# Kernel optimization log

Hardware: AMD Instinct MI355X
Metric: run time of the kernel (lower is better)

## Reference

```python
import jax, jax.numpy as jnp
import numpy as np

VOCAB = 32000
EMB = 256
HID = 1024
N = 5            # n-gram order
NM1 = N - 1      # context length
PAD = 0          # pad_index (ignore_index for CE, padding_idx for embedding)


def setup_inputs() -> dict:
    key = jax.random.key(0)
    ks = jax.random.split(key, 9)
    B, S = 16, 512
    text = jax.random.randint(ks[0], (B, S), 0, VOCAB)
    target = jax.random.randint(ks[1], (B, S), 0, VOCAB)
    sc = lambda fan_in: 1.0 / np.sqrt(fan_in)
    embed = jax.random.normal(ks[2], (VOCAB, EMB), jnp.float32) * 0.02
    W1 = jax.random.uniform(ks[3], (NM1 * EMB, HID), jnp.float32, -sc(NM1 * EMB), sc(NM1 * EMB))
    b1 = jax.random.uniform(ks[4], (HID,), jnp.float32, -sc(NM1 * EMB), sc(NM1 * EMB))
    W2 = jax.random.uniform(ks[5], (HID, HID), jnp.float32, -sc(HID), sc(HID))
    b2 = jax.random.uniform(ks[6], (HID,), jnp.float32, -sc(HID), sc(HID))
    Wo = jax.random.uniform(ks[7], (HID, VOCAB), jnp.float32, -sc(HID), sc(HID))
    bo = jax.random.uniform(ks[8], (VOCAB,), jnp.float32, -sc(HID), sc(HID))
    return {"text": text, "target": target, "embed": embed,
            "W1": W1, "b1": b1, "W2": W2, "b2": b2, "Wo": Wo, "bo": bo}


def reference(text, target, embed, W1, b1, W2, b2, Wo, bo):
    B, S = text.shape
    # left-pad with PAD so contexts[:, i] == previous n-1 tokens (padded for i < n-1)
    padded = jnp.pad(text, ((0, 0), (NM1, 0)), constant_values=PAD)  # [B, S+NM1]
    win = jnp.arange(S)[:, None] + jnp.arange(NM1)[None, :]          # [S, NM1]
    ctx = padded[:, win]                                             # [B, S, NM1]
    # nn.Embedding padding_idx: pad row is zero
    tab = embed.at[PAD].set(0.0)
    e = tab[ctx].reshape(B, S, NM1 * EMB)                            # [B, S, NM1*E]
    h1 = jax.nn.relu(jnp.einsum('bsd,dh->bsh', e, W1) + b1)
    h2 = jax.nn.relu(jnp.einsum('bsh,hk->bsk', h1, W2) + b2)
    logits = jnp.einsum('bsh,hv->bsv', h2, Wo) + bo                  # [B, S, V]
    logp = jax.nn.log_softmax(logits, axis=-1)
    nll = -jnp.take_along_axis(logp, target[..., None], axis=-1)[..., 0]  # [B, S]
    mask = (target != PAD).astype(logits.dtype)
    cnt = jnp.maximum(mask.sum(axis=0), 1.0)                         # per-timestep valid count
    step_loss = (nll * mask).sum(axis=0) / cnt                       # CE mean per step (ignore pad)
    return step_loss.mean()                                          # total_loss / seq_len
```

## Files before the change

kernel.cpp:

```cpp
#include <hip/hip_runtime.h>
#include <cstdint>
#include <cstddef>

#define VOCAB 32000
#define EMB   256
#define HID   1024
#define NB    16
#define SS    512
#define MTOK  (NB*SS)
#define KDIM  1024
#define NCHUNK 500
#define PSTRIDE 512
#define LOG2E 1.4426950408889634f
#define LN2   0.6931471805599453f

typedef float  f32x16 __attribute__((ext_vector_type(16)));
typedef int    i32x4  __attribute__((ext_vector_type(4)));
typedef int    i32x8  __attribute__((ext_vector_type(8)));

__device__ __forceinline__ float exp2_fast(float x) {
  float r; asm("v_exp_f32 %0, %1" : "=v"(r) : "v"(x)); return r;
}

__device__ __forceinline__ uint8_t f32_to_e4m3(float x) {
  union { float f; uint32_t u; } v; v.f = x;
  uint32_t s = (v.u >> 24) & 0x80u;
  int e = (int)((v.u >> 23) & 0xffu) - 127;
  uint32_t m = v.u & 0x7fffffu;
  if (e < -9) return (uint8_t)s;
  if (e >= -6) {
    uint32_t keep = m >> 20;
    uint32_t rest = m & 0xfffffu;
    keep += (rest > 0x80000u) || (rest == 0x80000u && (keep & 1u));
    if (keep == 8u) { keep = 0u; e += 1; }
    int code = ((e + 7) << 3) | (int)keep;
    if (code >= 0x7f) code = 0x7e;
    return (uint8_t)(s | (uint32_t)code);
  }
  uint32_t full = 0x800000u | m;
  int shift = 20 + (-6 - e);
  uint32_t keep = full >> shift;
  uint32_t rest = full & ((1u << shift) - 1u);
  uint32_t half = 1u << (shift - 1);
  keep += (rest > half) || (rest == half && (keep & 1u));
  if (keep >= 8u) return (uint8_t)(s | 0x08u);
  return (uint8_t)(s | keep);
}

__device__ __forceinline__ int f32_to_e2m1(float x) {
  int s = (x < 0.f) ? 8 : 0;
  float a = fabsf(x);
  int m;
  if      (a < 0.25f) m = 0;
  else if (a < 0.75f) m = 1;
  else if (a < 1.25f) m = 2;
  else if (a < 1.75f) m = 3;
  else if (a < 2.50f) m = 4;
  else if (a < 3.50f) m = 5;
  else if (a < 5.00f) m = 6;
  else                m = 7;
  return s | m;
}

__device__ __forceinline__ float e2m1_val(int c) {
  int m = c & 7;
  float mag = (m == 0) ? 0.0f : (m == 1) ? 0.5f : (m == 2) ? 1.0f :
              (m == 3) ? 1.5f : (m == 4) ? 2.0f : (m == 5) ? 3.0f :
              (m == 6) ? 4.0f : 6.0f;
  return (c & 8) ? -mag : mag;
}



__device__ __forceinline__ void w_frag8_body(const float* __restrict__ W,
                                             uint8_t* __restrict__ Bf, int C,
                                             int bx, int by, uint8_t* smem) {
  uint8_t (*tile)[128] = (uint8_t(*)[128])smem;
  const int v0 = bx * 128, k0 = by * 64;
  const int tid = threadIdx.x;
#pragma unroll
  for (int rr = 0; rr < 8; ++rr) {
    int row = rr * 8 + (tid >> 5);
    const float4 f = *(const float4*)&W[(size_t)(k0 + row) * C + v0 + (tid & 31) * 4];
    int vb = (tid & 31) * 4;
    tile[row][vb + 0] = f32_to_e4m3(f.x * 16.0f);
    tile[row][vb + 1] = f32_to_e4m3(f.y * 16.0f);
    tile[row][vb + 2] = f32_to_e4m3(f.z * 16.0f);
    tile[row][vb + 3] = f32_to_e4m3(f.w * 16.0f);
  }
  __syncthreads();
  const int rec = tid >> 6, l = tid & 63;
  const int vloc = rec * 32 + (l & 31);
  const int kb = (l >> 5) * 32;
  uint8_t* out = Bf + ((size_t)((bx * 4 + rec) * 16 + by)) * 2048 + l * 16;
  union { uint8_t b[16]; i32x4 v; } lo, hi;
#pragma unroll
  for (int j = 0; j < 16; ++j) {
    lo.b[j] = tile[kb + j][vloc];
    hi.b[j] = tile[kb + 16 + j][vloc];
  }
  *(i32x4*)(out)        = lo.v;
  *(i32x4*)(out + 1024) = hi.v;
}

__device__ __forceinline__ void wo_frag_body(const float* __restrict__ Wo,
                                             uint8_t* __restrict__ Bf,
                                             int bx, int by, uint8_t* smem) {
  uint8_t (*tile)[128] = (uint8_t(*)[128])smem;
  const int v0 = bx * 128, k0 = by * 64;
  const int tid = threadIdx.x;
  const float SC = 64.0f * LOG2E;
#pragma unroll
  for (int rr = 0; rr < 8; ++rr) {
    int row = rr * 8 + (tid >> 5);
    const float4 f = *(const float4*)&Wo[(size_t)(k0 + row) * VOCAB + v0 + (tid & 31) * 4];
    int vb = (tid & 31) * 4;
    tile[row][vb + 0] = (uint8_t)f32_to_e2m1(f.x * SC);
    tile[row][vb + 1] = (uint8_t)f32_to_e2m1(f.y * SC);
    tile[row][vb + 2] = (uint8_t)f32_to_e2m1(f.z * SC);
    tile[row][vb + 3] = (uint8_t)f32_to_e2m1(f.w * SC);
  }
  __syncthreads();
  const int rec = tid >> 6, l = tid & 63;
  const int vloc = rec * 32 + (l & 31);
  const int kb = (l >> 5) * 32;
  uint8_t* out = Bf + ((size_t)((bx * 4 + rec) * 16 + by)) * 1024 + l * 16;
  union { uint8_t b[16]; i32x4 v; } pk;
#pragma unroll
  for (int j = 0; j < 16; ++j)
    pk.b[j] = (uint8_t)(tile[kb + 2 * j][vloc] | (tile[kb + 2 * j + 1][vloc] << 4));
  *(i32x4*)(out) = pk.v;
}

__device__ __forceinline__ void gather_body(const int* __restrict__ text,
                                            const float* __restrict__ embed,
                                            uint8_t* __restrict__ Af,
                                            int rb, int jj) {
  const int sub = threadIdx.x >> 6, l = threadIdx.x & 63;
  const int kt = jj * 4 + sub;
  const int t = rb * 32 + (l & 31);
  const int b = t >> 9, s = t & 511;
  const int sidx = s + jj - 4;
  const int tok = (sidx >= 0) ? text[b * SS + sidx] : 0;
  uint8_t* out = Af + ((size_t)(rb * 16 + kt)) * 2048 + l * 16;
  if (tok == 0) {
    i32x4 z = {0, 0, 0, 0};
    *(i32x4*)(out) = z;
    *(i32x4*)(out + 1024) = z;
    return;
  }
  const int d0 = (kt & 3) * 64 + (l >> 5) * 32;
  const float* src = embed + (size_t)tok * EMB + d0;
  union { uint8_t b[16]; i32x4 v; } lo, hi;
#pragma unroll
  for (int q = 0; q < 4; ++q) {
    float4 f = *(const float4*)(src + q * 4);
    lo.b[q * 4 + 0] = f32_to_e4m3(f.x * 16.0f);
    lo.b[q * 4 + 1] = f32_to_e4m3(f.y * 16.0f);
    lo.b[q * 4 + 2] = f32_to_e4m3(f.z * 16.0f);
    lo.b[q * 4 + 3] = f32_to_e4m3(f.w * 16.0f);
    float4 g = *(const float4*)(src + 16 + q * 4);
    hi.b[q * 4 + 0] = f32_to_e4m3(g.x * 16.0f);
    hi.b[q * 4 + 1] = f32_to_e4m3(g.y * 16.0f);
    hi.b[q * 4 + 2] = f32_to_e4m3(g.z * 16.0f);
    hi.b[q * 4 + 3] = f32_to_e4m3(g.w * 16.0f);
  }
  *(i32x4*)(out)        = lo.v;
  *(i32x4*)(out + 1024) = hi.v;
}

__global__ __launch_bounds__(256)
void k_prep(const float* __restrict__ W1, const float* __restrict__ W2,
            const float* __restrict__ Wo, const float* __restrict__ bo,
            const int* __restrict__ text, const float* __restrict__ embed,
            uint8_t* __restrict__ W1Q, uint8_t* __restrict__ W2Q,
            uint8_t* __restrict__ WoQ, float* __restrict__ boP,
            uint8_t* __restrict__ EQ) {
  __shared__ uint8_t smem[64 * 128];
  int id = blockIdx.x;
  if (id < 128) { w_frag8_body(W1, W1Q, HID, id & 7, id >> 3, smem); return; }
  id -= 128;
  if (id < 128) { w_frag8_body(W2, W2Q, HID, id & 7, id >> 3, smem); return; }
  id -= 128;
  if (id < 4000) { wo_frag_body(Wo, WoQ, id % 250, id / 250, smem); return; }
  id -= 4000;
  if (id < 125) {
    int idx = id * 256 + threadIdx.x;
    int vb = idx >> 5, r = idx & 31;
    int kb = r >> 4, reg = r & 15;
    boP[idx] = bo[vb * 32 + (reg & 3) + 8 * (reg >> 2) + 4 * kb] * LOG2E;
    return;
  }
  id -= 125;
  gather_body(text, embed, EQ, id & 255, id >> 8);
}

template<int EPI>
__global__ __launch_bounds__(256, 2)
void k_gemm_mx8(const uint8_t* __restrict__ Af, const uint8_t* __restrict__ Bf,
                const float* __restrict__ bias, uint8_t* __restrict__ Hq) {
  const int tid  = threadIdx.x;
  const int lane = tid & 63, wid = tid >> 6;
  const int wm = wid >> 1, wn = wid & 1;
  const int lr = lane & 31;

  const int o   = blockIdx.x;
  const int xcd = o & 7, i = o >> 3;
  const int bm  = xcd * 8 + (i & 7);
  const int bn  = i >> 3;

  f32x16 acc[2][2];
#pragma unroll
  for (int m = 0; m < 2; ++m)
#pragma unroll
    for (int n = 0; n < 2; ++n)
#pragma unroll
      for (int e = 0; e < 16; ++e) acc[m][n][e] = 0.f;

  const uint8_t* pa0 = Af + ((size_t)(bm * 4 + wm * 2 + 0) * 16) * 2048 + lane * 16;
  const uint8_t* pa1 = Af + ((size_t)(bm * 4 + wm * 2 + 1) * 16) * 2048 + lane * 16;
  const uint8_t* pb0 = Bf + ((size_t)(bn * 4 + wn * 2 + 0) * 16) * 2048 + lane * 16;
  const uint8_t* pb1 = Bf + ((size_t)(bn * 4 + wn * 2 + 1) * 16) * 2048 + lane * 16;

#pragma unroll 1
  for (int kt = 0; kt < 16; ++kt) {
    i32x4 a0l = *(const i32x4*)(pa0), a0h = *(const i32x4*)(pa0 + 1024);
    i32x4 a1l = *(const i32x4*)(pa1), a1h = *(const i32x4*)(pa1 + 1024);
    i32x4 b0l = *(const i32x4*)(pb0), b0h = *(const i32x4*)(pb0 + 1024);
    i32x4 b1l = *(const i32x4*)(pb1), b1h = *(const i32x4*)(pb1 + 1024);
    pa0 += 2048; pa1 += 2048; pb0 += 2048; pb1 += 2048;

    i32x8 a0 = __builtin_shufflevector(a0l, a0h, 0, 1, 2, 3, 4, 5, 6, 7);
    i32x8 a1 = __builtin_shufflevector(a1l, a1h, 0, 1, 2, 3, 4, 5, 6, 7);
    i32x8 b0 = __builtin_shufflevector(b0l, b0h, 0, 1, 2, 3, 4, 5, 6, 7);
    i32x8 b1 = __builtin_shufflevector(b1l, b1h, 0, 1, 2, 3, 4, 5, 6, 7);

    __builtin_amdgcn_s_setprio(1);
    acc[0][0] = __builtin_amdgcn_mfma_scale_f32_32x32x64_f8f6f4(
        a0, b0, acc[0][0], 0, 0, 0, 123, 0, 123);
    acc[0][1] = __builtin_amdgcn_mfma_scale_f32_32x32x64_f8f6f4(
        a0, b1, acc[0][1], 0, 0, 0, 123, 0, 123);
    acc[1][0] = __builtin_amdgcn_mfma_scale_f32_32x32x64_f8f6f4(
        a1, b0, acc[1][0], 0, 0, 0, 123, 0, 123);
    acc[1][1] = __builtin_amdgcn_mfma_scale_f32_32x32x64_f8f6f4(
        a1, b1, acc[1][1], 0, 0, 0, 123, 0, 123);
    __builtin_amdgcn_s_setprio(0);
  }

  const int colbase = bn * 128 + wn * 64;
  const int recc = colbase >> 6;
  float bv0 = bias[colbase + lr];
  float bv1 = bias[colbase + 32 + lr];
#pragma unroll
  for (int m = 0; m < 2; ++m) {
#pragma unroll
    for (int reg = 0; reg < 16; ++reg) {
      int rowg = bm * 128 + wm * 64 + m * 32 + (reg & 3) + 8 * (reg >> 2) + 4 * (lane >> 5);
      float v0 = acc[m][0][reg] + bv0; v0 = v0 > 0.f ? v0 : 0.f;
      float v1 = acc[m][1][reg] + bv1; v1 = v1 > 0.f ? v1 : 0.f;
      size_t rec = (size_t)((rowg >> 5) * 16 + recc);
      if constexpr (EPI == 0) {
        size_t base = rec * 2048 + ((lr & 16) ? 1024 : 0) + (lr & 15);
        Hq[base + (size_t)(rowg & 31) * 16]        = f32_to_e4m3(v0 * 16.0f);
        Hq[base + (size_t)((rowg & 31) + 32) * 16] = f32_to_e4m3(v1 * 16.0f);
      } else {
        int q0 = f32_to_e2m1(v0 * 8.0f), q1 = f32_to_e2m1(v1 * 8.0f);
        int q0o = __shfl_xor(q0, 1), q1o = __shfl_xor(q1, 1);
        if ((lr & 1) == 0) {
          size_t base = rec * 1024 + (lr >> 1);
          Hq[base + (size_t)(rowg & 31) * 16]        = (uint8_t)(q0 | (q0o << 4));
          Hq[base + (size_t)((rowg & 31) + 32) * 16] = (uint8_t)(q1 | (q1o << 4));
        }
      }
    }
  }
}

__global__ __launch_bounds__(256, 2)
void k_gemm_vocab_mx(const uint8_t* __restrict__ Af,
                     const uint8_t* __restrict__ Bf,
                     const float* __restrict__ boP,
                     const int* __restrict__ target, const float* __restrict__ bo,
                     float* __restrict__ tlog,
                     float* __restrict__ psum) {
  if (blockIdx.x >= 16000) {
    const int r = (blockIdx.x - 16000) * 4 + (threadIdx.x >> 6);
    const int l = threadIdx.x & 63;
    const int tgt = target[r];
    const int ra = r >> 5, la = r & 31;
    const int rb = tgt >> 5, lb = tgt & 31;
    const int kt = l >> 2, half = (l & 2) ? 32 : 0, bofs = (l & 1) * 8;
    const uint8_t* pa = Bf + ((size_t)(ra * 16 + kt)) * 1024 + (la + half) * 16 + bofs;
    const uint8_t* pb = Af + ((size_t)(rb * 16 + kt)) * 1024 + (lb + half) * 16 + bofs;
    uint2 wa = *(const uint2*)pa;
    uint2 wb = *(const uint2*)pb;
    float s = 0.f;
#pragma unroll
    for (int j = 0; j < 8; ++j)
      s += e2m1_val((wa.x >> (4 * j)) & 0xF) * e2m1_val((wb.x >> (4 * j)) & 0xF);
#pragma unroll
    for (int j = 0; j < 8; ++j)
      s += e2m1_val((wa.y >> (4 * j)) & 0xF) * e2m1_val((wb.y >> (4 * j)) & 0xF);
#pragma unroll
    for (int st = 1; st < 64; st <<= 1) s += __shfl_xor(s, st);
    if (l == 0) tlog[r] = s * (1.0f / 512.0f) + bo[tgt] * LOG2E;
    return;
  }

  const int tid  = threadIdx.x;
  const int lane = tid & 63, wid = tid >> 6;
  const int wm = wid >> 1, wn = wid & 1;
  const int lr = lane & 31, kb = lane >> 5;

  const int t   = blockIdx.x;
  const int xcd = t & 7, i = t >> 3;
  const int bt  = xcd * 8 + (i & 7);
  const int bv  = i >> 3;

  f32x16 acc[2][2];
#pragma unroll
  for (int m = 0; m < 2; ++m)
#pragma unroll
    for (int n = 0; n < 2; ++n)
#pragma unroll
      for (int e = 0; e < 16; ++e) acc[m][n][e] = 0.f;

  const uint8_t* pa0 = Af + ((size_t)(bv * 4 + wm * 2 + 0) * 16) * 1024 + lane * 16;
  const uint8_t* pa1 = Af + ((size_t)(bv * 4 + wm * 2 + 1) * 16) * 1024 + lane * 16;
  const uint8_t* pb0 = Bf + ((size_t)(bt * 4 + wn * 2 + 0) * 16) * 1024 + lane * 16;
  const uint8_t* pb1 = Bf + ((size_t)(bt * 4 + wn * 2 + 1) * 16) * 1024 + lane * 16;

#pragma unroll 1
  for (int kt = 0; kt < 16; ++kt) {
    i32x4 a0q = *(const i32x4*)(pa0);
    i32x4 a1q = *(const i32x4*)(pa1);
    i32x4 b0q = *(const i32x4*)(pb0);
    i32x4 b1q = *(const i32x4*)(pb1);
    pa0 += 1024; pa1 += 1024; pb0 += 1024; pb1 += 1024;

    i32x8 a0 = __builtin_shufflevector(a0q, a0q, 0, 1, 2, 3, -1, -1, -1, -1);
    i32x8 a1 = __builtin_shufflevector(a1q, a1q, 0, 1, 2, 3, -1, -1, -1, -1);
    i32x8 b0 = __builtin_shufflevector(b0q, b0q, 0, 1, 2, 3, -1, -1, -1, -1);
    i32x8 b1 = __builtin_shufflevector(b1q, b1q, 0, 1, 2, 3, -1, -1, -1, -1);

    __builtin_amdgcn_s_setprio(1);
    acc[0][0] = __builtin_amdgcn_mfma_scale_f32_32x32x64_f8f6f4(
        a0, b0, acc[0][0], 4, 4, 0, 121, 0, 124);
    acc[0][1] = __builtin_amdgcn_mfma_scale_f32_32x32x64_f8f6f4(
        a0, b1, acc[0][1], 4, 4, 0, 121, 0, 124);
    acc[1][0] = __builtin_amdgcn_mfma_scale_f32_32x32x64_f8f6f4(
        a1, b0, acc[1][0], 4, 4, 0, 121, 0, 124);
    acc[1][1] = __builtin_amdgcn_mfma_scale_f32_32x32x64_f8f6f4(
        a1, b1, acc[1][1], 4, 4, 0, 121, 0, 124);
    __builtin_amdgcn_s_setprio(0);
  }

  const int chunk = bv * 2 + wm;
  const int tok0 = bt * 128 + wn * 64 + lr;
  const int tok1 = tok0 + 32;
  float s0 = 0.f, s1 = 0.f;
#pragma unroll
  for (int m = 0; m < 2; ++m) {
    const float4* bp = (const float4*)&boP[(size_t)((bv * 4 + wm * 2 + m) * 32 + kb * 16)];
    float4 q0 = bp[0], q1 = bp[1], q2 = bp[2], q3 = bp[3];
#define EPI4(Q, R0)                                                         \
    s0 += exp2_fast(acc[m][0][(R0) + 0] + Q.x);                             \
    s1 += exp2_fast(acc[m][1][(R0) + 0] + Q.x);                             \
    s0 += exp2_fast(acc[m][0][(R0) + 1] + Q.y);                             \
    s1 += exp2_fast(acc[m][1][(R0) + 1] + Q.y);                             \
    s0 += exp2_fast(acc[m][0][(R0) + 2] + Q.z);                             \
    s1 += exp2_fast(acc[m][1][(R0) + 2] + Q.z);                             \
    s0 += exp2_fast(acc[m][0][(R0) + 3] + Q.w);                             \
    s1 += exp2_fast(acc[m][1][(R0) + 3] + Q.w);
    EPI4(q0, 0)
    EPI4(q1, 4)
    EPI4(q2, 8)
    EPI4(q3, 12)
#undef EPI4
  }
  s0 += __shfl_xor(s0, 32);
  s1 += __shfl_xor(s1, 32);
  if (kb == 0) {
    psum[(size_t)tok0 * PSTRIDE + chunk] = s0;
    psum[(size_t)tok1 * PSTRIDE + chunk] = s1;
  }
}

__global__ void k_reduce_nll(const float* __restrict__ psum,
                             const float* __restrict__ tlog,
                             float* __restrict__ nll) {
  int row = blockIdx.x;
  int lane = threadIdx.x;
  float L = 0.f;
  for (int ch = lane; ch < NCHUNK; ch += 64)
    L += psum[(size_t)row * PSTRIDE + ch];
#pragma unroll
  for (int s = 1; s < 64; s <<= 1) L += __shfl_xor(L, s);
  if (lane == 0) nll[row] = LN2 * (log2f(L) - tlog[row]);
}

__global__ void k_loss(const int* __restrict__ target,
                       const float* __restrict__ nll,
                       float* __restrict__ out) {
  __shared__ float red[SS];
  int s = threadIdx.x;
  float sl = 0.f, cnt = 0.f;
#pragma unroll
  for (int b = 0; b < NB; ++b) {
    int idx = b * SS + s;
    if (target[idx] != 0) { sl += nll[idx]; cnt += 1.f; }
  }
  red[s] = sl / fmaxf(cnt, 1.f);
  __syncthreads();
  for (int st = 256; st > 0; st >>= 1) {
    if (s < st) red[s] += red[s + st];
    __syncthreads();
  }
  if (s == 0) out[0] = red[0] / (float)SS;
}

extern "C" void kernel_launch(void* const* d_in, const int* in_sizes, int n_in,
                              void* d_out, int out_size, void* d_ws, size_t ws_size,
                              hipStream_t stream) {
  (void)in_sizes; (void)n_in; (void)out_size; (void)ws_size;
  const int*   text   = (const int*)d_in[0];
  const int*   target = (const int*)d_in[1];
  const float* embed  = (const float*)d_in[2];
  const float* W1     = (const float*)d_in[3];
  const float* b1     = (const float*)d_in[4];
  const float* W2     = (const float*)d_in[5];
  const float* b2     = (const float*)d_in[6];
  const float* Wo     = (const float*)d_in[7];
  const float* bo     = (const float*)d_in[8];
  float* out = (float*)d_out;
  char* ws = (char*)d_ws;

  char* p = ws;
  uint8_t* EQ  = (uint8_t*)p; p += (size_t)MTOK * KDIM;
  uint8_t* H1Q = (uint8_t*)p; p += (size_t)MTOK * HID;
  uint8_t* H2Q = (uint8_t*)p; p += (size_t)MTOK * HID / 2;
  uint8_t* W1Q = (uint8_t*)p; p += (size_t)HID * HID;
  uint8_t* W2Q = (uint8_t*)p; p += (size_t)HID * HID;
  uint8_t* WoQ = (uint8_t*)p; p += (size_t)VOCAB * HID / 2;
  float* boP  = (float*)p;    p += (size_t)VOCAB * 4;
  float* psum = (float*)p;    p += (size_t)MTOK * PSTRIDE * 4;
  float* tlog = (float*)p;    p += (size_t)MTOK * 4;
  float* nll  = (float*)p;

  k_prep<<<5405, 256, 0, stream>>>(W1, W2, Wo, bo, text, embed,
                                   W1Q, W2Q, WoQ, boP, EQ);

  k_gemm_mx8<0><<<dim3((MTOK / 128) * (HID / 128)), 256, 0, stream>>>(EQ, W1Q, b1, H1Q);
  k_gemm_mx8<1><<<dim3((MTOK / 128) * (HID / 128)), 256, 0, stream>>>(H1Q, W2Q, b2, H2Q);

  k_gemm_vocab_mx<<<dim3(16000 + MTOK / 4), 256, 0, stream>>>(
      WoQ, H2Q, boP, target, bo, tlog, psum);

  k_reduce_nll<<<MTOK, 64, 0, stream>>>(psum, tlog, nll);
  k_loss<<<1, SS, 0, stream>>>(target, nll, out);
}
```

Before: 262.0 us.

## Overlap Wo quantization with FFN GEMMs and fuse final loss reduction via atomics

The Wo weight quantization (4000 blocks) moves out of the prep kernel and is split across the two FFN GEMM launches as extra trailing blocks, so it runs alongside the matmuls instead of serializing before them. The prep kernel now gathers embeddings first and also precomputes per-timestep reciprocal valid counts. The separate nll and loss kernels are merged into one reduction that atomically adds weighted per-token NLL into the output, dropping a launch and the single-block tree reduction. In exchange the float atomics make the sum order nondeterministic, and the GEMM kernels now declare extra shared memory that may affect occupancy.

```diff
diff --git a/kernel.cpp b/kernel.cpp
--- a/kernel.cpp
+++ b/kernel.cpp
@@ -69,7 +69,6 @@
               (m == 6) ? 4.0f : 6.0f;
   return (c & 8) ? -mag : mag;
 }
-
 
 
 __device__ __forceinline__ void w_frag8_body(const float* __restrict__ W,
@@ -170,20 +169,21 @@
 }
 
 __global__ __launch_bounds__(256)
-void k_prep(const float* __restrict__ W1, const float* __restrict__ W2,
-            const float* __restrict__ Wo, const float* __restrict__ bo,
-            const int* __restrict__ text, const float* __restrict__ embed,
-            uint8_t* __restrict__ W1Q, uint8_t* __restrict__ W2Q,
-            uint8_t* __restrict__ WoQ, float* __restrict__ boP,
-            uint8_t* __restrict__ EQ) {
+void k_prep_a(const float* __restrict__ W1, const float* __restrict__ W2,
+              const float* __restrict__ bo,
+              const int* __restrict__ text, const int* __restrict__ target,
+              const float* __restrict__ embed,
+              uint8_t* __restrict__ W1Q, uint8_t* __restrict__ W2Q,
+              float* __restrict__ boP, float* __restrict__ rcnt,
+              uint8_t* __restrict__ EQ, float* __restrict__ out) {
   __shared__ uint8_t smem[64 * 128];
   int id = blockIdx.x;
+  if (id < 1024) { gather_body(text, embed, EQ, id & 255, id >> 8); return; }
+  id -= 1024;
   if (id < 128) { w_frag8_body(W1, W1Q, HID, id & 7, id >> 3, smem); return; }
   id -= 128;
   if (id < 128) { w_frag8_body(W2, W2Q, HID, id & 7, id >> 3, smem); return; }
   id -= 128;
-  if (id < 4000) { wo_frag_body(Wo, WoQ, id % 250, id / 250, smem); return; }
-  id -= 4000;
   if (id < 125) {
     int idx = id * 256 + threadIdx.x;
     int vb = idx >> 5, r = idx & 31;
@@ -192,13 +192,25 @@
     return;
   }
   id -= 125;
-  gather_body(text, embed, EQ, id & 255, id >> 8);
-}
-
-template<int EPI>
+  int s = id * 256 + threadIdx.x;
+  int cnt = 0;
+#pragma unroll
+  for (int b = 0; b < NB; ++b) cnt += (target[b * SS + s] != 0) ? 1 : 0;
+  rcnt[s] = 1.0f / ((float)(cnt > 0 ? cnt : 1) * (float)SS);
+  if (id == 0 && threadIdx.x == 0) out[0] = 0.0f;
+}
+
+template<int EPI, int WOHALF>
 __global__ __launch_bounds__(256, 2)
-void k_gemm_mx8(const uint8_t* __restrict__ Af, const uint8_t* __restrict__ Bf,
-                const float* __restrict__ bias, uint8_t* __restrict__ Hq) {
+void k_ffn_wo(const uint8_t* __restrict__ Af, const uint8_t* __restrict__ Bf,
+              const float* __restrict__ bias, uint8_t* __restrict__ Hq,
+              const float* __restrict__ Wo, uint8_t* __restrict__ WoQ) {
+  __shared__ uint8_t smem[64 * 128];
+  if (blockIdx.x >= 512) {
+    int wid2 = (blockIdx.x - 512) + WOHALF * 2000;
+    wo_frag_body(Wo, WoQ, wid2 % 250, wid2 / 250, smem);
+    return;
+  }
   const int tid  = threadIdx.x;
   const int lane = tid & 63, wid = tid >> 6;
   const int wm = wid >> 1, wn = wid & 1;
@@ -386,9 +398,11 @@
   }
 }
 
-__global__ void k_reduce_nll(const float* __restrict__ psum,
-                             const float* __restrict__ tlog,
-                             float* __restrict__ nll) {
+__global__ void k_reduce_loss(const float* __restrict__ psum,
+                              const float* __restrict__ tlog,
+                              const int* __restrict__ target,
+                              const float* __restrict__ rcnt,
+                              float* __restrict__ out) {
   int row = blockIdx.x;
   int lane = threadIdx.x;
   float L = 0.f;
@@ -396,27 +410,10 @@
     L += psum[(size_t)row * PSTRIDE + ch];
 #pragma unroll
   for (int s = 1; s < 64; s <<= 1) L += __shfl_xor(L, s);
-  if (lane == 0) nll[row] = LN2 * (log2f(L) - tlog[row]);
-}
-
-__global__ void k_loss(const int* __restrict__ target,
-                       const float* __restrict__ nll,
-                       float* __restrict__ out) {
-  __shared__ float red[SS];
-  int s = threadIdx.x;
-  float sl = 0.f, cnt = 0.f;
-#pragma unroll
-  for (int b = 0; b < NB; ++b) {
-    int idx = b * SS + s;
-    if (target[idx] != 0) { sl += nll[idx]; cnt += 1.f; }
-  }
-  red[s] = sl / fmaxf(cnt, 1.f);
-  __syncthreads();
-  for (int st = 256; st > 0; st >>= 1) {
-    if (s < st) red[s] += red[s + st];
-    __syncthreads();
-  }
-  if (s == 0) out[0] = red[0] / (float)SS;
+  if (lane == 0 && target[row] != 0) {
+    float nll = LN2 * (log2f(L) - tlog[row]);
+    atomicAdd(out, nll * rcnt[row & 511]);
+  }
 }
 
 extern "C" void kernel_launch(void* const* d_in, const int* in_sizes, int n_in,
@@ -443,19 +440,18 @@
   uint8_t* W2Q = (uint8_t*)p; p += (size_t)HID * HID;
   uint8_t* WoQ = (uint8_t*)p; p += (size_t)VOCAB * HID / 2;
   float* boP  = (float*)p;    p += (size_t)VOCAB * 4;
+  float* rcnt = (float*)p;    p += (size_t)SS * 4;
   float* psum = (float*)p;    p += (size_t)MTOK * PSTRIDE * 4;
   float* tlog = (float*)p;    p += (size_t)MTOK * 4;
-  float* nll  = (float*)p;
-
-  k_prep<<<5405, 256, 0, stream>>>(W1, W2, Wo, bo, text, embed,
-                                   W1Q, W2Q, WoQ, boP, EQ);
-
-  k_gemm_mx8<0><<<dim3((MTOK / 128) * (HID / 128)), 256, 0, stream>>>(EQ, W1Q, b1, H1Q);
-  k_gemm_mx8<1><<<dim3((MTOK / 128) * (HID / 128)), 256, 0, stream>>>(H1Q, W2Q, b2, H2Q);
+
+  k_prep_a<<<1407, 256, 0, stream>>>(W1, W2, bo, text, target, embed,
+                                     W1Q, W2Q, boP, rcnt, EQ, out);
+
+  k_ffn_wo<0, 0><<<2512, 256, 0, stream>>>(EQ, W1Q, b1, H1Q, Wo, WoQ);
+  k_ffn_wo<1, 1><<<2512, 256, 0, stream>>>(H1Q, W2Q, b2, H2Q, Wo, WoQ);
 
   k_gemm_vocab_mx<<<dim3(16000 + MTOK / 4), 256, 0, stream>>>(
       WoQ, H2Q, boP, target, bo, tlog, psum);
 
-  k_reduce_nll<<<MTOK, 64, 0, stream>>>(psum, tlog, nll);
-  k_loss<<<1, SS, 0, stream>>>(target, nll, out);
-}
+  k_reduce_loss<<<MTOK, 64, 0, stream>>>(psum, tlog, target, rcnt, out);
+}
```

Result: slower. 353.1 us (+34.8%).
